# Kernel optimization log

Hardware: AMD Instinct MI355X
Metric: run time of the kernel (lower is better)

Reference implementation:

```python
import jax, jax.numpy as jnp
import numpy as np

B, H, W, DIM = 8, 128, 128, 96
MED = 2 * DIM            # med_channels
NS = 3                   # num_scales
SCTX = 48                # spatial context channels
RIN = DIM + SCTX         # reweight mlp input
RHID = int(0.25 * RIN)   # 36
ROUT = NS * MED          # 576
FH, FWH = H, W // 2 + 1  # rfft2 output grid
SCALE_HW = [(16, 9), (8, 4), (24, 13)]  # per-scale filter resolutions


def _cubic(t, a=-0.75):
    t = abs(t)
    if t <= 1.0:
        return (a + 2) * t ** 3 - (a + 3) * t ** 2 + 1.0
    if t < 2.0:
        return a * t ** 3 - 5 * a * t ** 2 + 8 * a * t - 4 * a
    return 0.0


def _resize_mat(old, new):
    # bicubic, align_corners=True, border replication (matches F.interpolate)
    M = np.zeros((new, old), dtype=np.float32)
    for j in range(new):
        s = j * (old - 1) / (new - 1) if new > 1 else 0.0
        f = int(np.floor(s))
        for k in range(-1, 3):
            M[j, min(max(f + k, 0), old - 1)] += _cubic(s - (f + k))
    return jnp.asarray(M)


def _soa(x, scale, bias):
    r = jnp.maximum(x, 0.0)
    return scale * r * r + bias


def setup_inputs() -> dict:
    key = jax.random.key(0)
    ks = jax.random.split(key, 10)
    inp = {
        "x": jax.random.normal(ks[0], (B, H, W, DIM), dtype=jnp.float32),
        "w1": jax.random.normal(ks[1], (MED, DIM), dtype=jnp.float32) * 0.02,
        "soa1_scale": jnp.ones((1,), jnp.float32),
        "soa1_bias": jnp.zeros((1,), jnp.float32),
        "cw0": jax.random.normal(ks[2], (SCALE_HW[0][0], SCALE_HW[0][1], MED, 2), dtype=jnp.float32) * 0.02,
        "cw1": jax.random.normal(ks[3], (SCALE_HW[1][0], SCALE_HW[1][1], MED, 2), dtype=jnp.float32) * 0.02,
        "cw2": jax.random.normal(ks[4], (SCALE_HW[2][0], SCALE_HW[2][1], MED, 2), dtype=jnp.float32) * 0.02,
        "sp_w": jax.random.normal(ks[5], (SCTX, DIM), dtype=jnp.float32) * 0.05,
        "bn_gamma": jnp.ones((SCTX,), jnp.float32),
        "bn_beta": jnp.zeros((SCTX,), jnp.float32),
        "bn_mean": jnp.zeros((SCTX,), jnp.float32),
        "bn_var": jnp.ones((SCTX,), jnp.float32),
        "fc1": jax.random.normal(ks[6], (RHID, RIN), dtype=jnp.float32) * 0.05,
        "mlp_scale": jnp.ones((1,), jnp.float32),
        "mlp_bias": jnp.zeros((1,), jnp.float32),
        "fc2": jax.random.normal(ks[7], (ROUT, RHID), dtype=jnp.float32) * 0.05,
        "w2": jax.random.normal(ks[8], (DIM, MED), dtype=jnp.float32) * 0.02,
    }
    return inp


def reference(x, w1, soa1_scale, soa1_bias, cw0, cw1, cw2, sp_w,
              bn_gamma, bn_beta, bn_mean, bn_var,
              fc1, mlp_scale, mlp_bias, fc2, w2):
    # pwconv1 + Soa act
    x_pre = _soa(jnp.einsum('bhwc,mc->bhwm', x, w1), soa1_scale, soa1_bias)
    # rfft2 over spatial dims (ortho) -> [B, FH, FWH, MED] complex64
    xf = jnp.fft.rfft2(x_pre.transpose(0, 3, 1, 2), axes=(2, 3), norm='ortho').transpose(0, 2, 3, 1)
    # resize each scale's complex weight to the fft grid (bicubic align_corners=True)
    filts = []
    for cw in (cw0, cw1, cw2):
        Rh = _resize_mat(cw.shape[0], FH)
        Rw = _resize_mat(cw.shape[1], FWH)
        t = jnp.einsum('Hh,hwmc->Hwmc', Rh, cw)
        t = jnp.einsum('Ww,Hwmc->HWmc', Rw, t)
        filts.append(jax.lax.complex(t[..., 0], t[..., 1]))
    filt = jnp.stack(filts)  # [NS, FH, FWH, MED] complex64
    # routing context: global channel mean + 1x1 conv / BN(eval) / relu / GAP
    gctx = x.mean(axis=(1, 2))  # [B, DIM]
    y = jnp.einsum('bhwc,sc->bhws', x, sp_w)
    y = (y - bn_mean) * jax.lax.rsqrt(bn_var + 1e-5) * bn_gamma + bn_beta
    sctx = jnp.maximum(y, 0.0).mean(axis=(1, 2))  # [B, SCTX]
    fused = jnp.concatenate([gctx, sctx], axis=1)  # [B, RIN]
    hmid = _soa(fused @ fc1.T, mlp_scale, mlp_bias)
    r = jax.nn.softmax((hmid @ fc2.T).reshape(-1, NS, MED), axis=1)  # [B, NS, MED]
    # routing-weighted combined filter + spectral multiply
    comb = jnp.einsum('shwm,bsm->bhwm', filt, r.astype(filt.dtype))
    xff = xf * comb
    xsp = jnp.fft.irfft2(xff.transpose(0, 3, 1, 2), s=(H, W), axes=(2, 3), norm='ortho').transpose(0, 2, 3, 1)
    # act2 is Identity; pwconv2
    return jnp.einsum('bhwm,cm->bhwc', xsp, w2)
```

## Files before the change

kernel.cpp:

```cpp
#include <hip/hip_runtime.h>
#include <math.h>

#define BB    8
#define HH    128
#define WW    128
#define DIM   96
#define MED   192
#define HWPX  16384
#define PSTR  16672
#define FWH   65
#define LSTR  67

#define P_OFF     0
#define P_SZ      (8*192*PSTR)
#define FILT_OFF  (P_OFF + P_SZ)
#define FILT_SZ   (3*192*128*65*2)
#define PART_OFF  (FILT_OFF + FILT_SZ)
#define PART_SZ   (8*144*256)
#define R_OFF     (PART_OFF + PART_SZ)
#define W1B_OFF   (R_OFF + 4608)
#define W2B_OFF   (W1B_OFF + 23040)

typedef __attribute__((ext_vector_type(8))) short short8_t;
typedef __attribute__((ext_vector_type(4))) float float4_t;

__device__ __forceinline__ unsigned short bf16_rne(float f){
  unsigned u = __float_as_uint(f);
  unsigned r = (u + 0x7FFFu + ((u>>16)&1u)) >> 16;
  return (unsigned short)r;
}
__device__ __forceinline__ float bf16_to_f(unsigned short h){
  return __uint_as_float(((unsigned)h) << 16);
}

__device__ __forceinline__ float cubicw(float tt){
  float t = fabsf(tt), t2=t*t, t3=t2*t;
  if (t <= 1.f) return 1.25f*t3 - 2.25f*t2 + 1.f;
  if (t < 2.f)  return -0.75f*t3 + 3.75f*t2 - 6.f*t + 3.f;
  return 0.f;
}

__global__ __launch_bounds__(256) void k_prep_filt(
    const float* __restrict__ w1, const float* __restrict__ sp_w,
    const float* __restrict__ w2,
    const float* __restrict__ cw0, const float* __restrict__ cw1,
    const float* __restrict__ cw2,
    unsigned short* __restrict__ W1B, unsigned short* __restrict__ W2B,
    float* __restrict__ filt)
{
  __shared__ float2 T[128][13];
  int bx = blockIdx.x;
  int t = threadIdx.x;

  if (bx < 36) {
    int tid = t + bx*256;
    int nthr = 256*36;
    for (int i = tid; i < 2*3*15*512; i += nthr) {
      int j = i & 7, l = (i>>3) & 63;
      int nt = (i>>9) % 15, kc = ((i>>9)/15) % 3, term = i / (3*15*512);
      int r = nt*16 + (l&15);
      int c = kc*32 + (l>>4)*8 + j;
      float v = (r < 192) ? w1[r*96 + c] : sp_w[(r-192)*96 + c];
      unsigned short hi = bf16_rne(v);
      W1B[i] = (term==0) ? hi : bf16_rne(v - bf16_to_f(hi));
    }
    for (int i = tid; i < 2*6*6*512; i += nthr) {
      int j = i & 7, l = (i>>3) & 63;
      int nt = (i>>9) % 6, kc = ((i>>9)/6) % 6, term = i / (6*6*512);
      int cp = nt*16 + (l&15);
      int m  = kc*32 + (l>>4)*8 + j;
      float v = w2[cp*192 + m];
      unsigned short hi = bf16_rne(v);
      W2B[i] = (term==0) ? hi : bf16_rne(v - bf16_to_f(hi));
    }
    return;
  }

  int fb = bx - 36;
  int s = fb / 192, m = fb - s*192;
  const float* cw = (s==0) ? cw0 : ((s==1) ? cw1 : cw2);
  const int SH = (s==0) ? 16 : ((s==1) ? 8 : 24);
  const int SW = (s==0) ? 9  : ((s==1) ? 4 : 13);

  for (int i = t; i < 128*SW; i += 256) {
    int fh = i / SW, iw = i - fh*SW;
    float sh = fh * (float)(SH-1) / 127.f;
    int fh0 = (int)floorf(sh);
    float2 acc = make_float2(0.f, 0.f);
    #pragma unroll
    for (int ka=0; ka<4; ++ka) {
      int kk = fh0-1+ka;
      float w = cubicw(sh - (float)kk);
      int ih = min(max(kk,0), SH-1);
      float2 v = *(const float2*)(cw + (size_t)((ih*SW + iw)*192 + m)*2);
      acc.x = fmaf(w, v.x, acc.x);
      acc.y = fmaf(w, v.y, acc.y);
    }
    T[fh][iw] = acc;
  }
  __syncthreads();

  float2* outp = (float2*)filt + (size_t)(s*192+m)*8320;
  for (int i = t; i < 128*65; i += 256) {
    int fh = i / 65, fw = i - fh*65;
    float sw = fw * (float)(SW-1) / 64.f;
    int fw0 = (int)floorf(sw);
    float2 acc = make_float2(0.f, 0.f);
    #pragma unroll
    for (int kb=0; kb<4; ++kb) {
      int jj = fw0-1+kb;
      float w = cubicw(sw - (float)jj);
      int iw = min(max(jj,0), SW-1);
      float2 v = T[fh][iw];
      acc.x = fmaf(w, v.x, acc.x);
      acc.y = fmaf(w, v.y, acc.y);
    }
    outp[i] = acc;
  }
}

__global__ __launch_bounds__(256) void k_pw1(
    const float* __restrict__ x, const unsigned short* __restrict__ W1B,
    const float* __restrict__ soa_scale, const float* __restrict__ soa_bias,
    const float* __restrict__ bn_gamma, const float* __restrict__ bn_beta,
    const float* __restrict__ bn_mean, const float* __restrict__ bn_var,
    float* __restrict__ P, float* __restrict__ part)
{
  __shared__ float red[4][144];
  __shared__ float bnA_s[48], bnB_s[48];
  int t = threadIdx.x;
  int lane = t & 63, wv = t >> 6;
  if (t < 48) {
    float a = bn_gamma[t] * rsqrtf(bn_var[t] + 1e-5f);
    bnA_s[t] = a; bnB_s[t] = bn_beta[t] - bn_mean[t]*a;
  }
  int blk = blockIdx.x;
  int px0 = blk*64 + wv*16;
  int b = (blk*64) >> 14;
  int pxl = px0 & 16383;
  int g = lane >> 4;

  float4_t acc[15];
  #pragma unroll
  for (int nt=0; nt<15; ++nt) acc[nt] = (float4_t){0.f,0.f,0.f,0.f};

  #pragma unroll
  for (int kc=0; kc<3; ++kc) {
    const float* xp = x + (size_t)(px0 + (lane&15))*96 + kc*32 + g*8;
    float4 v0 = *(const float4*)xp;
    float4 v1 = *(const float4*)(xp+4);
    float vv[8] = {v0.x,v0.y,v0.z,v0.w, v1.x,v1.y,v1.z,v1.w};
    #pragma unroll
    for (int j=0;j<8;j++){
      float s = vv[j];
      s += __shfl_xor(s, 1);
      s += __shfl_xor(s, 2);
      s += __shfl_xor(s, 4);
      s += __shfl_xor(s, 8);
      if ((lane & 15) == 0) red[wv][kc*32 + g*8 + j] = s;
    }
    short8_t Bh, Bl;
    #pragma unroll
    for (int j=0;j<8;j++){
      unsigned short h = bf16_rne(vv[j]);
      Bh[j] = (short)h;
      Bl[j] = (short)bf16_rne(vv[j] - bf16_to_f(h));
    }
    const short8_t* a_hi = (const short8_t*)(W1B + (size_t)(0*3+kc)*15*512) + lane;
    const short8_t* a_lo = (const short8_t*)(W1B + (size_t)(1*3+kc)*15*512) + lane;
    #pragma unroll
    for (int nt=0; nt<15; ++nt) {
      short8_t Ah = a_hi[nt*64];
      short8_t Al = a_lo[nt*64];
      acc[nt] = __builtin_amdgcn_mfma_f32_16x16x32_bf16(Ah, Bh, acc[nt], 0,0,0);
      acc[nt] = __builtin_amdgcn_mfma_f32_16x16x32_bf16(Ah, Bl, acc[nt], 0,0,0);
      acc[nt] = __builtin_amdgcn_mfma_f32_16x16x32_bf16(Al, Bh, acc[nt], 0,0,0);
    }
  }
  float sc = soa_scale[0], bi = soa_bias[0];
  #pragma unroll
  for (int nt=0; nt<12; ++nt) {
    #pragma unroll
    for (int q=0;q<4;q++){
      float d = acc[nt][q];
      float v = fmaxf(d, 0.f);
      d = sc*v*v + bi;
      int mp = nt*16 + g*4 + q;
      P[(size_t)(b*192 + mp)*PSTR + pxl + (lane&15)] = d;
    }
  }
  #pragma unroll
  for (int tile=0; tile<3; ++tile) {
    #pragma unroll
    for (int q=0;q<4;q++){
      int s = tile*16 + g*4 + q;
      float y = acc[12+tile][q];
      float v = fmaxf(bnA_s[s]*y + bnB_s[s], 0.f);
      v += __shfl_xor(v, 1);
      v += __shfl_xor(v, 2);
      v += __shfl_xor(v, 4);
      v += __shfl_xor(v, 8);
      if ((lane & 15) == 0) red[wv][96 + s] = v;
    }
  }
  __syncthreads();
  if (t < 144) {
    float s = red[0][t] + red[1][t] + red[2][t] + red[3][t];
    part[((size_t)(b*144) + t)*256 + (blk & 255)] = s;
  }
}

__global__ __launch_bounds__(256) void k_pw2(
    const float* __restrict__ P, const unsigned short* __restrict__ W2B,
    float* __restrict__ out)
{
  int t = threadIdx.x;
  int lane = t & 63, wv = t >> 6;
  int px0 = blockIdx.x*64 + wv*16;
  int b = px0 >> 14;
  int pxl = px0 & 16383;

  float4_t acc[6];
  #pragma unroll
  for (int nt=0; nt<6; ++nt) acc[nt] = (float4_t){0.f,0.f,0.f,0.f};

  #pragma unroll
  for (int kc=0; kc<6; ++kc) {
    const float* ap = P + (size_t)(b*192 + kc*32 + (lane>>4)*8)*PSTR + pxl + (lane&15);
    short8_t Ah, Al;
    #pragma unroll
    for (int j=0;j<8;j++){
      float v = ap[(size_t)j*PSTR];
      unsigned short h = bf16_rne(v);
      Ah[j] = (short)h;
      Al[j] = (short)bf16_rne(v - bf16_to_f(h));
    }
    const short8_t* b_hi = (const short8_t*)(W2B + (size_t)(0*6+kc)*6*512) + lane;
    const short8_t* b_lo = (const short8_t*)(W2B + (size_t)(1*6+kc)*6*512) + lane;
    #pragma unroll
    for (int nt=0; nt<6; ++nt) {
      short8_t Bh = b_hi[nt*64];
      short8_t Bl = b_lo[nt*64];
      acc[nt] = __builtin_amdgcn_mfma_f32_16x16x32_bf16(Ah, Bh, acc[nt], 0,0,0);
      acc[nt] = __builtin_amdgcn_mfma_f32_16x16x32_bf16(Ah, Bl, acc[nt], 0,0,0);
      acc[nt] = __builtin_amdgcn_mfma_f32_16x16x32_bf16(Al, Bh, acc[nt], 0,0,0);
    }
  }
  #pragma unroll
  for (int nt=0; nt<6; ++nt) {
    #pragma unroll
    for (int q=0;q<4;q++){
      int px = px0 + (lane>>4)*4 + q;
      out[(size_t)px*96 + nt*16 + (lane&15)] = acc[nt][q];
    }
  }
}

__global__ __launch_bounds__(256) void k_route2(
    const float* __restrict__ part,
    const float* __restrict__ fc1, const float* __restrict__ fc2,
    const float* __restrict__ mlp_scale, const float* __restrict__ mlp_bias,
    float* __restrict__ r_out)
{
  __shared__ float fused[144], hmid[36], rpre[576];
  int t = threadIdx.x, b = blockIdx.x;
  if (t < 144) {
    const float* pp = part + ((size_t)(b*144) + t)*256;
    float s = 0.f;
    for (int i = 0; i < 256; i += 4) {
      float4 v = *(const float4*)(pp + i);
      s += (v.x + v.y) + (v.z + v.w);
    }
    fused[t] = s * (1.f/16384.f);
  }
  __syncthreads();
  if (t < 36) {
    float a = 0.f;
    for (int i=0;i<144;i++) a = fmaf(fused[i], fc1[t*144+i], a);
    float rr = fmaxf(a, 0.f);
    hmid[t] = mlp_scale[0]*rr*rr + mlp_bias[0];
  }
  __syncthreads();
  for (int o = t; o < 576; o += 256) {
    float a = 0.f;
    for (int j=0;j<36;j++) a = fmaf(hmid[j], fc2[o*36+j], a);
    rpre[o] = a;
  }
  __syncthreads();
  if (t < 192) {
    float v0 = rpre[t], v1 = rpre[192+t], v2 = rpre[384+t];
    float mx = fmaxf(v0, fmaxf(v1, v2));
    float e0 = expf(v0-mx), e1 = expf(v1-mx), e2 = expf(v2-mx);
    float inv = 1.f/(e0+e1+e2);
    r_out[(b*3+0)*192+t] = e0*inv;
    r_out[(b*3+1)*192+t] = e1*inv;
    r_out[(b*3+2)*192+t] = e2*inv;
  }
}

__device__ __forceinline__ float2 c_add(float2 a, float2 b){ return make_float2(a.x+b.x, a.y+b.y); }
__device__ __forceinline__ float2 c_sub(float2 a, float2 b){ return make_float2(a.x-b.x, a.y-b.y); }
__device__ __forceinline__ float2 c_mul(float2 a, float2 w){ return make_float2(a.x*w.x - a.y*w.y, a.x*w.y + a.y*w.x); }
__device__ __forceinline__ float2 c_mulc(float2 a, float2 w){ return make_float2(a.x*w.x + a.y*w.y, a.y*w.x - a.x*w.y); }

__device__ __forceinline__ void dif4(float2* S, const float2* TW,
    int a0, int a1, int a2, int a3, int t1, int t2, int t3)
{
  float2 x0=S[a0], x1=S[a1], x2=S[a2], x3=S[a3];
  float2 u = c_add(x0,x2), d0 = c_sub(x0,x2);
  float2 s = c_add(x1,x3), d1 = c_sub(x1,x3);
  float2 w = c_mul(d0, TW[t1]);
  float2 v = c_mul(d1, TW[t2]);
  float2 t3w = TW[t3];
  S[a0] = c_add(u,s);
  S[a1] = c_mul(c_sub(u,s), t3w);
  S[a2] = c_add(w,v);
  S[a3] = c_mul(c_sub(w,v), t3w);
}

__device__ __forceinline__ void dit4(float2* S, const float2* TW,
    int a0, int a1, int a2, int a3, int tA, int tB, int tC)
{
  float2 x0=S[a0], x1=S[a1], x2=S[a2], x3=S[a3];
  float2 wA = TW[tA];
  float2 x1t = c_mulc(x1, wA), x3t = c_mulc(x3, wA);
  float2 u = c_add(x0,x1t), v = c_sub(x0,x1t);
  float2 s = c_add(x2,x3t), w = c_sub(x2,x3t);
  float2 st = c_mulc(s, TW[tB]);
  float2 wt = c_mulc(w, TW[tC]);
  S[a0] = c_add(u, st);
  S[a2] = c_sub(u, st);
  S[a1] = c_add(v, wt);
  S[a3] = c_sub(v, wt);
}

__global__ __launch_bounds__(512, 4) void k_spectral(
    float* __restrict__ P, const float* __restrict__ filt, const float* __restrict__ r)
{
  __shared__ float2 S[128*LSTR];
  __shared__ float2 TW[64];
  int t = threadIdx.x;
  int lane = t & 63, wid = t >> 6;

  int i = blockIdx.x;
  int b = (i >> 3) & 7;
  int m = (i & 7) * 24 + (i >> 6);
  float* plane = P + ((size_t)b*192 + m) * PSTR;

  {
    float ang = -6.283185307179586477f * (float)lane / 128.f;
    TW[lane] = make_float2(cosf(ang), sinf(ang));
  }

  for (int it = 0; it < 8; ++it) {
    int row = 16*wid + (lane>>5) + 2*it;
    int j   = lane & 31;
    float4 v = ((const float4*)plane)[row*32 + j];
    int base = row*LSTR + 2*j;
    S[base]   = make_float2(v.x, v.y);
    S[base+1] = make_float2(v.z, v.w);
  }
  float r0 = r[(b*3+0)*192+m];
  float r1 = r[(b*3+1)*192+m];
  float r2 = r[(b*3+2)*192+m];

  #pragma unroll
  for (int ps = 0; ps < 3; ++ps) {
    const int lh = 5 - 2*ps;
    const int h1 = 1 << lh, h2 = h1 >> 1;
    #pragma unroll
    for (int it = 0; it < 4; ++it) {
      int g = lane & 15;
      int row = 16*wid + (lane>>4) + 4*it;
      int k = g & (h2-1), blk = g >> (lh-1);
      int base = row*LSTR + blk*(2*h1) + k;
      dif4(S,TW, base, base+h2, base+h1, base+h1+h2,
           k << (6-lh), (k+h2) << (6-lh), k << (7-lh));
    }
  }

  for (int it = 0; it < 9; ++it) {
    int k   = (lane>>4) + 4*it;
    int row = 16*wid + (lane & 15);
    if (k <= 32) {
      int base = row*LSTR;
      if (k == 0) {
        float2 z = S[base];
        S[base]    = make_float2(z.x + z.y, 0.f);
        S[base+64] = make_float2(z.x - z.y, 0.f);
      } else {
        int a = __brev((unsigned)k) >> 26;
        int bidx = __brev((unsigned)(64-k)) >> 26;
        float2 A = S[base+a], B = S[base+bidx];
        float sr_ = 0.5f*(A.x+B.x), si_ = 0.5f*(A.y-B.y);
        float dr  = 0.5f*(A.x-B.x), di  = 0.5f*(A.y+B.y);
        float2 wq = TW[k];
        float tr = wq.x*di + wq.y*dr;
        float ti = -(wq.x*dr - wq.y*di);
        S[base+a]    = make_float2(sr_ + tr,  si_ + ti);
        S[base+bidx] = make_float2(sr_ - tr, -si_ + ti);
      }
    }
  }
  __syncthreads();

  #pragma unroll
  for (int ps = 0; ps < 3; ++ps) {
    const int lh = 6 - 2*ps;
    const int h1 = 1 << lh, h2 = h1 >> 1;
    for (int it = 0; it < 5; ++it) {
      int idx = t + 512*it;
      if (idx < 65*32) {
        int g = idx / 65, col = idx - g*65;
        int k = g & (h2-1), blk = g >> (lh-1);
        int p = blk*(2*h1) + k;
        dif4(S,TW, p*LSTR+col, (p+h2)*LSTR+col, (p+h1)*LSTR+col, (p+h1+h2)*LSTR+col,
             k << (6-lh), (k+h2) << (6-lh), k << (7-lh));
      }
    }
    __syncthreads();
  }

  {
    const float2* fb0 = (const float2*)filt + (size_t)(0*192+m)*8320;
    const float2* fb1 = (const float2*)filt + (size_t)(1*192+m)*8320;
    const float2* fb2 = (const float2*)filt + (size_t)(2*192+m)*8320;
    const float inv = 1.f/8192.f;
    for (int it = 0; it < 9; ++it) {
      int idx = t + 512*it;
      if (idx < 65*64) {
        int f = idx / 65, fw = idx - f*65;
        int j = __brev((unsigned)f) >> 26;
        int cc = (fw == 64) ? 64 : (__brev((unsigned)fw) >> 26);
        int a0 = (2*j)*LSTR + cc, a1 = a0 + LSTR;
        float2 u = S[a0], v = S[a1];
        float2 e = c_add(u,v), o = c_sub(u,v);
        float2 f00=fb0[idx],      f10=fb1[idx],      f20=fb2[idx];
        float2 f01=fb0[idx+4160], f11=fb1[idx+4160], f21=fb2[idx+4160];
        float cr0 = (r0*f00.x + r1*f10.x + r2*f20.x) * inv;
        float ci0 = (r0*f00.y + r1*f10.y + r2*f20.y) * inv;
        float cr1 = (r0*f01.x + r1*f11.x + r2*f21.x) * inv;
        float ci1 = (r0*f01.y + r1*f11.y + r2*f21.y) * inv;
        S[a0] = make_float2(e.x*cr0 - e.y*ci0, e.x*ci0 + e.y*cr0);
        S[a1] = make_float2(o.x*cr1 - o.y*ci1, o.x*ci1 + o.y*cr1);
      }
    }
  }
  __syncthreads();

  #pragma unroll
  for (int ps = 0; ps < 3; ++ps) {
    const int la = 2*ps;
    const int h = 1 << la;
    for (int it = 0; it < 5; ++it) {
      int idx = t + 512*it;
      if (idx < 65*32) {
        int g = idx / 65, col = idx - g*65;
        int k = g & (h-1), blk = g >> la;
        int p = blk*(4*h) + k;
        dit4(S,TW, p*LSTR+col, (p+h)*LSTR+col, (p+2*h)*LSTR+col, (p+3*h)*LSTR+col,
             k << (6-la), k << (5-la), (k+h) << (5-la));
      }
    }
    __syncthreads();
  }
  for (int it = 0; it < 9; ++it) {
    int idx = t + 512*it;
    if (idx < 65*64) {
      int k = idx / 65, col = idx - k*65;
      int a0 = k*LSTR + col, a1 = a0 + 64*LSTR;
      float2 u = S[a0], xv = S[a1];
      float2 xt = c_mulc(xv, TW[k]);
      S[a0] = c_add(u,xt); S[a1] = c_sub(u,xt);
    }
  }
  __syncthreads();

  for (int it = 0; it < 9; ++it) {
    int k   = (lane>>4) + 4*it;
    int row = 16*wid + (lane & 15);
    if (k <= 32) {
      int base = row*LSTR;
      if (k == 0) {
        float ar = S[base].x;
        float cr = S[base+64].x;
        S[base] = make_float2(0.5f*(ar+cr), 0.5f*(ar-cr));
      } else {
        int a = __brev((unsigned)k) >> 26;
        int bidx = __brev((unsigned)(64-k)) >> 26;
        float2 A = S[base+a], B = S[base+bidx];
        float sr_ = 0.5f*(A.x+B.x), si_ = 0.5f*(A.y-B.y);
        float dr  = 0.5f*(A.x-B.x), di  = 0.5f*(A.y+B.y);
        float2 wq = TW[k];
        float tr2 = wq.y*dr - wq.x*di;
        float ti2 = wq.x*dr + wq.y*di;
        S[base+a]    = make_float2(sr_ + tr2,  si_ + ti2);
        S[base+bidx] = make_float2(sr_ - tr2, -si_ + ti2);
      }
    }
  }

  #pragma unroll
  for (int ps = 0; ps < 3; ++ps) {
    const int la = 2*ps;
    const int h = 1 << la;
    #pragma unroll
    for (int it = 0; it < 4; ++it) {
      int g = lane & 15;
      int row = 16*wid + (lane>>4) + 4*it;
      int k = g & (h-1), blk = g >> la;
      int base = row*LSTR + blk*(4*h) + k;
      dit4(S,TW, base, base+h, base+2*h, base+3*h,
           k << (6-la), k << (5-la), (k+h) << (5-la));
    }
  }

  for (int it = 0; it < 8; ++it) {
    int row = 16*wid + (lane>>5) + 2*it;
    int j   = lane & 31;
    int base = row*LSTR + 2*j;
    float2 z0 = S[base], z1 = S[base+1];
    float4 v; v.x = z0.x; v.y = z0.y; v.z = z1.x; v.w = z1.y;
    ((float4*)plane)[row*32 + j] = v;
  }
}

extern "C" void kernel_launch(void* const* d_in, const int* in_sizes, int n_in,
                              void* d_out, int out_size, void* d_ws, size_t ws_size,
                              hipStream_t stream) {
  const float* x          = (const float*)d_in[0];
  const float* w1         = (const float*)d_in[1];
  const float* soa1_scale = (const float*)d_in[2];
  const float* soa1_bias  = (const float*)d_in[3];
  const float* cw0        = (const float*)d_in[4];
  const float* cw1        = (const float*)d_in[5];
  const float* cw2        = (const float*)d_in[6];
  const float* sp_w       = (const float*)d_in[7];
  const float* bn_gamma   = (const float*)d_in[8];
  const float* bn_beta    = (const float*)d_in[9];
  const float* bn_mean    = (const float*)d_in[10];
  const float* bn_var     = (const float*)d_in[11];
  const float* fc1        = (const float*)d_in[12];
  const float* mlp_scale  = (const float*)d_in[13];
  const float* mlp_bias   = (const float*)d_in[14];
  const float* fc2        = (const float*)d_in[15];
  const float* w2         = (const float*)d_in[16];
  float* out = (float*)d_out;

  float* ws   = (float*)d_ws;
  float* P    = ws + P_OFF;
  float* filt = ws + FILT_OFF;
  float* part = ws + PART_OFF;
  float* rbuf = ws + R_OFF;
  unsigned short* W1B = (unsigned short*)(ws + W1B_OFF);
  unsigned short* W2B = (unsigned short*)(ws + W2B_OFF);

  k_prep_filt<<<612, 256, 0, stream>>>(w1, sp_w, w2, cw0, cw1, cw2, W1B, W2B, filt);
  k_pw1      <<<2048,256, 0, stream>>>(x, W1B, soa1_scale, soa1_bias,
                                       bn_gamma, bn_beta, bn_mean, bn_var,
                                       P, part);
  k_route2   <<<8,   256, 0, stream>>>(part, fc1, fc2, mlp_scale, mlp_bias, rbuf);
  k_spectral <<<1536,512, 0, stream>>>(P, filt, rbuf);
  k_pw2      <<<2048,256, 0, stream>>>(P, W2B, out);
}
```

Baseline: 359.2 us.

## Split pw1 output channels across wave pairs and fuse routing MLP via last-block counter

The pw1 kernel now processes 32 pixels per block, with two waves per 16-pixel group each computing half of the 15 output tiles. This halves per-wave accumulator registers and doubles the grid, aiming for better occupancy. The separate routing kernel is removed: each block bumps an atomic counter and the last 8 blocks to finish run the routing MLP and softmax, one per batch image. This saves a launch but adds an atomic and threadfences per block. Correctness relies on the last-8 blocks seeing all partials, which is only guaranteed for the final block, so there is a possible ordering race.

```diff
diff --git a/kernel.cpp b/kernel.cpp
--- a/kernel.cpp
+++ b/kernel.cpp
@@ -11,15 +11,18 @@
 #define FWH   65
 #define LSTR  67
 
+#define PW1_GRID 4096
+
 #define P_OFF     0
 #define P_SZ      (8*192*PSTR)
 #define FILT_OFF  (P_OFF + P_SZ)
 #define FILT_SZ   (3*192*128*65*2)
 #define PART_OFF  (FILT_OFF + FILT_SZ)
-#define PART_SZ   (8*144*256)
+#define PART_SZ   (8*144*512)
 #define R_OFF     (PART_OFF + PART_SZ)
 #define W1B_OFF   (R_OFF + 4608)
 #define W2B_OFF   (W1B_OFF + 23040)
+#define CNT_OFF   (W2B_OFF + 18432)
 
 typedef __attribute__((ext_vector_type(8))) short short8_t;
 typedef __attribute__((ext_vector_type(4))) float float4_t;
@@ -46,13 +49,14 @@
     const float* __restrict__ cw0, const float* __restrict__ cw1,
     const float* __restrict__ cw2,
     unsigned short* __restrict__ W1B, unsigned short* __restrict__ W2B,
-    float* __restrict__ filt)
+    float* __restrict__ filt, int* __restrict__ cnt)
 {
   __shared__ float2 T[128][13];
   int bx = blockIdx.x;
   int t = threadIdx.x;
 
   if (bx < 36) {
+    if (bx == 0 && t == 0) *cnt = 0;
     int tid = t + bx*256;
     int nthr = 256*36;
     for (int i = tid; i < 2*3*15*512; i += nthr) {
@@ -124,25 +128,29 @@
     const float* __restrict__ soa_scale, const float* __restrict__ soa_bias,
     const float* __restrict__ bn_gamma, const float* __restrict__ bn_beta,
     const float* __restrict__ bn_mean, const float* __restrict__ bn_var,
-    float* __restrict__ P, float* __restrict__ part)
+    float* __restrict__ P, float* __restrict__ part, int* __restrict__ cnt,
+    const float* __restrict__ fc1, const float* __restrict__ fc2,
+    const float* __restrict__ mlp_scale, const float* __restrict__ mlp_bias,
+    float* __restrict__ r_out)
 {
-  __shared__ float red[4][144];
+  __shared__ float red[2][144];
   __shared__ float bnA_s[48], bnB_s[48];
   int t = threadIdx.x;
   int lane = t & 63, wv = t >> 6;
+  int pg = wv >> 1, h = wv & 1;
   if (t < 48) {
     float a = bn_gamma[t] * rsqrtf(bn_var[t] + 1e-5f);
     bnA_s[t] = a; bnB_s[t] = bn_beta[t] - bn_mean[t]*a;
   }
   int blk = blockIdx.x;
-  int px0 = blk*64 + wv*16;
-  int b = (blk*64) >> 14;
+  int px0 = blk*32 + pg*16;
+  int b = (blk*32) >> 14;
   int pxl = px0 & 16383;
   int g = lane >> 4;
 
-  float4_t acc[15];
-  #pragma unroll
-  for (int nt=0; nt<15; ++nt) acc[nt] = (float4_t){0.f,0.f,0.f,0.f};
+  float4_t acc[8];
+  #pragma unroll
+  for (int nt=0; nt<8; ++nt) acc[nt] = (float4_t){0.f,0.f,0.f,0.f};
 
   #pragma unroll
   for (int kc=0; kc<3; ++kc) {
@@ -150,63 +158,133 @@
     float4 v0 = *(const float4*)xp;
     float4 v1 = *(const float4*)(xp+4);
     float vv[8] = {v0.x,v0.y,v0.z,v0.w, v1.x,v1.y,v1.z,v1.w};
+    if (h == 0) {
+      #pragma unroll
+      for (int j=0;j<8;j++){
+        float s = vv[j];
+        s += __shfl_xor(s, 1);
+        s += __shfl_xor(s, 2);
+        s += __shfl_xor(s, 4);
+        s += __shfl_xor(s, 8);
+        if ((lane & 15) == 0) red[pg][kc*32 + g*8 + j] = s;
+      }
+    }
+    short8_t Bh, Bl;
     #pragma unroll
     for (int j=0;j<8;j++){
-      float s = vv[j];
-      s += __shfl_xor(s, 1);
-      s += __shfl_xor(s, 2);
-      s += __shfl_xor(s, 4);
-      s += __shfl_xor(s, 8);
-      if ((lane & 15) == 0) red[wv][kc*32 + g*8 + j] = s;
-    }
-    short8_t Bh, Bl;
-    #pragma unroll
-    for (int j=0;j<8;j++){
-      unsigned short h = bf16_rne(vv[j]);
-      Bh[j] = (short)h;
-      Bl[j] = (short)bf16_rne(vv[j] - bf16_to_f(h));
+      unsigned short hh = bf16_rne(vv[j]);
+      Bh[j] = (short)hh;
+      Bl[j] = (short)bf16_rne(vv[j] - bf16_to_f(hh));
     }
     const short8_t* a_hi = (const short8_t*)(W1B + (size_t)(0*3+kc)*15*512) + lane;
     const short8_t* a_lo = (const short8_t*)(W1B + (size_t)(1*3+kc)*15*512) + lane;
-    #pragma unroll
-    for (int nt=0; nt<15; ++nt) {
-      short8_t Ah = a_hi[nt*64];
-      short8_t Al = a_lo[nt*64];
-      acc[nt] = __builtin_amdgcn_mfma_f32_16x16x32_bf16(Ah, Bh, acc[nt], 0,0,0);
-      acc[nt] = __builtin_amdgcn_mfma_f32_16x16x32_bf16(Ah, Bl, acc[nt], 0,0,0);
-      acc[nt] = __builtin_amdgcn_mfma_f32_16x16x32_bf16(Al, Bh, acc[nt], 0,0,0);
+    if (h == 0) {
+      #pragma unroll
+      for (int nt=0; nt<8; ++nt) {
+        short8_t Ah = a_hi[nt*64];
+        short8_t Al = a_lo[nt*64];
+        acc[nt] = __builtin_amdgcn_mfma_f32_16x16x32_bf16(Ah, Bh, acc[nt], 0,0,0);
+        acc[nt] = __builtin_amdgcn_mfma_f32_16x16x32_bf16(Ah, Bl, acc[nt], 0,0,0);
+        acc[nt] = __builtin_amdgcn_mfma_f32_16x16x32_bf16(Al, Bh, acc[nt], 0,0,0);
+      }
+    } else {
+      #pragma unroll
+      for (int nt=0; nt<7; ++nt) {
+        short8_t Ah = a_hi[(nt+8)*64];
+        short8_t Al = a_lo[(nt+8)*64];
+        acc[nt] = __builtin_amdgcn_mfma_f32_16x16x32_bf16(Ah, Bh, acc[nt], 0,0,0);
+        acc[nt] = __builtin_amdgcn_mfma_f32_16x16x32_bf16(Ah, Bl, acc[nt], 0,0,0);
+        acc[nt] = __builtin_amdgcn_mfma_f32_16x16x32_bf16(Al, Bh, acc[nt], 0,0,0);
+      }
     }
   }
   float sc = soa_scale[0], bi = soa_bias[0];
-  #pragma unroll
-  for (int nt=0; nt<12; ++nt) {
-    #pragma unroll
-    for (int q=0;q<4;q++){
-      float d = acc[nt][q];
-      float v = fmaxf(d, 0.f);
-      d = sc*v*v + bi;
-      int mp = nt*16 + g*4 + q;
-      P[(size_t)(b*192 + mp)*PSTR + pxl + (lane&15)] = d;
-    }
-  }
-  #pragma unroll
-  for (int tile=0; tile<3; ++tile) {
-    #pragma unroll
-    for (int q=0;q<4;q++){
-      int s = tile*16 + g*4 + q;
-      float y = acc[12+tile][q];
-      float v = fmaxf(bnA_s[s]*y + bnB_s[s], 0.f);
-      v += __shfl_xor(v, 1);
-      v += __shfl_xor(v, 2);
-      v += __shfl_xor(v, 4);
-      v += __shfl_xor(v, 8);
-      if ((lane & 15) == 0) red[wv][96 + s] = v;
+  if (h == 0) {
+    #pragma unroll
+    for (int nt=0; nt<8; ++nt) {
+      #pragma unroll
+      for (int q=0;q<4;q++){
+        float d = acc[nt][q];
+        float v = fmaxf(d, 0.f);
+        d = sc*v*v + bi;
+        int mp = nt*16 + g*4 + q;
+        P[(size_t)(b*192 + mp)*PSTR + pxl + (lane&15)] = d;
+      }
+    }
+  } else {
+    #pragma unroll
+    for (int nt=0; nt<4; ++nt) {
+      #pragma unroll
+      for (int q=0;q<4;q++){
+        float d = acc[nt][q];
+        float v = fmaxf(d, 0.f);
+        d = sc*v*v + bi;
+        int mp = (nt+8)*16 + g*4 + q;
+        P[(size_t)(b*192 + mp)*PSTR + pxl + (lane&15)] = d;
+      }
+    }
+    #pragma unroll
+    for (int tile=0; tile<3; ++tile) {
+      #pragma unroll
+      for (int q=0;q<4;q++){
+        int s = tile*16 + g*4 + q;
+        float y = acc[4+tile][q];
+        float v = fmaxf(bnA_s[s]*y + bnB_s[s], 0.f);
+        v += __shfl_xor(v, 1);
+        v += __shfl_xor(v, 2);
+        v += __shfl_xor(v, 4);
+        v += __shfl_xor(v, 8);
+        if ((lane & 15) == 0) red[pg][96 + s] = v;
+      }
     }
   }
   __syncthreads();
   if (t < 144) {
-    float s = red[0][t] + red[1][t] + red[2][t] + red[3][t];
-    part[((size_t)(b*144) + t)*256 + (blk & 255)] = s;
+    float s = red[0][t] + red[1][t];
+    part[((size_t)(b*144) + t)*512 + (blk & 511)] = s;
+  }
+
+  __threadfence();
+  __shared__ int sidx;
+  if (t == 0) sidx = atomicAdd(cnt, 1);
+  __syncthreads();
+  int idx = sidx;
+  if (idx < PW1_GRID - 8) return;
+  __threadfence();
+  int b2 = idx - (PW1_GRID - 8);
+
+  __shared__ float fused[144], hmid[36], rpre[576];
+  if (t < 144) {
+    const float* pp = part + ((size_t)(b2*144) + t)*512;
+    float s = 0.f;
+    for (int i = 0; i < 512; i += 4) {
+      float4 v = *(const float4*)(pp + i);
+      s += (v.x + v.y) + (v.z + v.w);
+    }
+    fused[t] = s * (1.f/16384.f);
+  }
+  __syncthreads();
+  if (t < 36) {
+    float a = 0.f;
+    for (int i=0;i<144;i++) a = fmaf(fused[i], fc1[t*144+i], a);
+    float rr = fmaxf(a, 0.f);
+    hmid[t] = mlp_scale[0]*rr*rr + mlp_bias[0];
+  }
+  __syncthreads();
+  for (int o = t; o < 576; o += 256) {
+    float a = 0.f;
+    for (int j=0;j<36;j++) a = fmaf(hmid[j], fc2[o*36+j], a);
+    rpre[o] = a;
+  }
+  __syncthreads();
+  if (t < 192) {
+    float v0 = rpre[t], v1 = rpre[192+t], v2 = rpre[384+t];
+    float mx = fmaxf(v0, fmaxf(v1, v2));
+    float e0 = expf(v0-mx), e1 = expf(v1-mx), e2 = expf(v2-mx);
+    float inv = 1.f/(e0+e1+e2);
+    r_out[(b2*3+0)*192+t] = e0*inv;
+    r_out[(b2*3+1)*192+t] = e1*inv;
+    r_out[(b2*3+2)*192+t] = e2*inv;
   }
 }
 
@@ -253,48 +331,6 @@
       int px = px0 + (lane>>4)*4 + q;
       out[(size_t)px*96 + nt*16 + (lane&15)] = acc[nt][q];
     }
-  }
-}
-
-__global__ __launch_bounds__(256) void k_route2(
-    const float* __restrict__ part,
-    const float* __restrict__ fc1, const float* __restrict__ fc2,
-    const float* __restrict__ mlp_scale, const float* __restrict__ mlp_bias,
-    float* __restrict__ r_out)
-{
-  __shared__ float fused[144], hmid[36], rpre[576];
-  int t = threadIdx.x, b = blockIdx.x;
-  if (t < 144) {
-    const float* pp = part + ((size_t)(b*144) + t)*256;
-    float s = 0.f;
-    for (int i = 0; i < 256; i += 4) {
-      float4 v = *(const float4*)(pp + i);
-      s += (v.x + v.y) + (v.z + v.w);
-    }
-    fused[t] = s * (1.f/16384.f);
-  }
-  __syncthreads();
-  if (t < 36) {
-    float a = 0.f;
-    for (int i=0;i<144;i++) a = fmaf(fused[i], fc1[t*144+i], a);
-    float rr = fmaxf(a, 0.f);
-    hmid[t] = mlp_scale[0]*rr*rr + mlp_bias[0];
-  }
-  __syncthreads();
-  for (int o = t; o < 576; o += 256) {
-    float a = 0.f;
-    for (int j=0;j<36;j++) a = fmaf(hmid[j], fc2[o*36+j], a);
-    rpre[o] = a;
-  }
-  __syncthreads();
-  if (t < 192) {
-    float v0 = rpre[t], v1 = rpre[192+t], v2 = rpre[384+t];
-    float mx = fmaxf(v0, fmaxf(v1, v2));
-    float e0 = expf(v0-mx), e1 = expf(v1-mx), e2 = expf(v2-mx);
-    float inv = 1.f/(e0+e1+e2);
-    r_out[(b*3+0)*192+t] = e0*inv;
-    r_out[(b*3+1)*192+t] = e1*inv;
-    r_out[(b*3+2)*192+t] = e2*inv;
   }
 }
 
@@ -554,12 +590,13 @@
   float* rbuf = ws + R_OFF;
   unsigned short* W1B = (unsigned short*)(ws + W1B_OFF);
   unsigned short* W2B = (unsigned short*)(ws + W2B_OFF);
-
-  k_prep_filt<<<612, 256, 0, stream>>>(w1, sp_w, w2, cw0, cw1, cw2, W1B, W2B, filt);
-  k_pw1      <<<2048,256, 0, stream>>>(x, W1B, soa1_scale, soa1_bias,
-                                       bn_gamma, bn_beta, bn_mean, bn_var,
-                                       P, part);
-  k_route2   <<<8,   256, 0, stream>>>(part, fc1, fc2, mlp_scale, mlp_bias, rbuf);
+  int* cnt = (int*)(ws + CNT_OFF);
+
+  k_prep_filt<<<612, 256, 0, stream>>>(w1, sp_w, w2, cw0, cw1, cw2, W1B, W2B, filt, cnt);
+  k_pw1      <<<PW1_GRID, 256, 0, stream>>>(x, W1B, soa1_scale, soa1_bias,
+                                            bn_gamma, bn_beta, bn_mean, bn_var,
+                                            P, part, cnt,
+                                            fc1, fc2, mlp_scale, mlp_bias, rbuf);
   k_spectral <<<1536,512, 0, stream>>>(P, filt, rbuf);
   k_pw2      <<<2048,256, 0, stream>>>(P, W2B, out);
 }
```

Result: slower. 939.9 us (+161.7%).

## Assign FFT columns to fixed waves and drop column-FFT barriers; repack filter layout

Applied to the files above, without the earlier changes.

Column FFT passes (DIF, spectral multiply, DIT) now give each wave its own 8 columns, with the extra column 64 handled by wave 0. All of a column's butterflies therefore stay inside one wave, and the __syncthreads between passes are removed. The filter bake writes a bit-reversed, column-major float4 layout so each thread loads both spectral halves with one vector load. Relying on intra-wave ordering without barriers depends on wave-level execution semantics. Wave 0 also carries extra work for the odd column, which imbalances the waves.

```diff
diff --git a/kernel.cpp b/kernel.cpp
--- a/kernel.cpp
+++ b/kernel.cpp
@@ -14,7 +14,7 @@
 #define P_OFF     0
 #define P_SZ      (8*192*PSTR)
 #define FILT_OFF  (P_OFF + P_SZ)
-#define FILT_SZ   (3*192*128*65*2)
+#define FILT_SZ   (3*192*65*64*4)
 #define PART_OFF  (FILT_OFF + FILT_SZ)
 #define PART_SZ   (8*144*256)
 #define R_OFF     (PART_OFF + PART_SZ)
@@ -100,22 +100,28 @@
   }
   __syncthreads();
 
-  float2* outp = (float2*)filt + (size_t)(s*192+m)*8320;
-  for (int i = t; i < 128*65; i += 256) {
-    int fh = i / 65, fw = i - fh*65;
+  float4* outp = (float4*)filt + (size_t)(s*192+m)*4160;
+  for (int i = t; i < 65*64; i += 256) {
+    int cc = i >> 6, j = i & 63;
+    int f  = __brev((unsigned)j) >> 26;
+    int fw = (cc == 64) ? 64 : (__brev((unsigned)cc) >> 26);
     float sw = fw * (float)(SW-1) / 64.f;
     int fw0 = (int)floorf(sw);
-    float2 acc = make_float2(0.f, 0.f);
+    float2 a0 = make_float2(0.f, 0.f);
+    float2 a1 = make_float2(0.f, 0.f);
     #pragma unroll
     for (int kb=0; kb<4; ++kb) {
       int jj = fw0-1+kb;
       float w = cubicw(sw - (float)jj);
       int iw = min(max(jj,0), SW-1);
-      float2 v = T[fh][iw];
-      acc.x = fmaf(w, v.x, acc.x);
-      acc.y = fmaf(w, v.y, acc.y);
-    }
-    outp[i] = acc;
+      float2 v0 = T[f][iw];
+      float2 v1 = T[f+64][iw];
+      a0.x = fmaf(w, v0.x, a0.x);
+      a0.y = fmaf(w, v0.y, a0.y);
+      a1.x = fmaf(w, v1.x, a1.x);
+      a1.y = fmaf(w, v1.y, a1.y);
+    }
+    outp[i] = make_float4(a0.x, a0.y, a1.x, a1.y);
   }
 }
 
@@ -404,75 +410,100 @@
   }
   __syncthreads();
 
+  int cs = lane & 7, u8 = lane >> 3;
+  int mycol = 8*wid + cs;
+
   #pragma unroll
   for (int ps = 0; ps < 3; ++ps) {
     const int lh = 6 - 2*ps;
     const int h1 = 1 << lh, h2 = h1 >> 1;
-    for (int it = 0; it < 5; ++it) {
-      int idx = t + 512*it;
-      if (idx < 65*32) {
-        int g = idx / 65, col = idx - g*65;
-        int k = g & (h2-1), blk = g >> (lh-1);
-        int p = blk*(2*h1) + k;
-        dif4(S,TW, p*LSTR+col, (p+h2)*LSTR+col, (p+h1)*LSTR+col, (p+h1+h2)*LSTR+col,
-             k << (6-lh), (k+h2) << (6-lh), k << (7-lh));
-      }
-    }
-    __syncthreads();
+    #pragma unroll
+    for (int it = 0; it < 4; ++it) {
+      int bf = 8*it + u8;
+      int k = bf & (h2-1), blk = bf >> (lh-1);
+      int p = blk*(2*h1) + k;
+      dif4(S,TW, p*LSTR+mycol, (p+h2)*LSTR+mycol, (p+h1)*LSTR+mycol, (p+h1+h2)*LSTR+mycol,
+           k << (6-lh), (k+h2) << (6-lh), k << (7-lh));
+    }
+    if (wid == 0 && lane < 32) {
+      int bf = lane;
+      int k = bf & (h2-1), blk = bf >> (lh-1);
+      int p = blk*(2*h1) + k;
+      dif4(S,TW, p*LSTR+64, (p+h2)*LSTR+64, (p+h1)*LSTR+64, (p+h1+h2)*LSTR+64,
+           k << (6-lh), (k+h2) << (6-lh), k << (7-lh));
+    }
   }
 
   {
-    const float2* fb0 = (const float2*)filt + (size_t)(0*192+m)*8320;
-    const float2* fb1 = (const float2*)filt + (size_t)(1*192+m)*8320;
-    const float2* fb2 = (const float2*)filt + (size_t)(2*192+m)*8320;
+    const float4* fb0 = (const float4*)filt + (size_t)(0*192+m)*4160;
+    const float4* fb1 = (const float4*)filt + (size_t)(1*192+m)*4160;
+    const float4* fb2 = (const float4*)filt + (size_t)(2*192+m)*4160;
     const float inv = 1.f/8192.f;
-    for (int it = 0; it < 9; ++it) {
-      int idx = t + 512*it;
-      if (idx < 65*64) {
-        int f = idx / 65, fw = idx - f*65;
-        int j = __brev((unsigned)f) >> 26;
-        int cc = (fw == 64) ? 64 : (__brev((unsigned)fw) >> 26);
-        int a0 = (2*j)*LSTR + cc, a1 = a0 + LSTR;
-        float2 u = S[a0], v = S[a1];
-        float2 e = c_add(u,v), o = c_sub(u,v);
-        float2 f00=fb0[idx],      f10=fb1[idx],      f20=fb2[idx];
-        float2 f01=fb0[idx+4160], f11=fb1[idx+4160], f21=fb2[idx+4160];
-        float cr0 = (r0*f00.x + r1*f10.x + r2*f20.x) * inv;
-        float ci0 = (r0*f00.y + r1*f10.y + r2*f20.y) * inv;
-        float cr1 = (r0*f01.x + r1*f11.x + r2*f21.x) * inv;
-        float ci1 = (r0*f01.y + r1*f11.y + r2*f21.y) * inv;
-        S[a0] = make_float2(e.x*cr0 - e.y*ci0, e.x*ci0 + e.y*cr0);
-        S[a1] = make_float2(o.x*cr1 - o.y*ci1, o.x*ci1 + o.y*cr1);
-      }
-    }
-  }
-  __syncthreads();
+    #pragma unroll
+    for (int it = 0; it < 8; ++it) {
+      int j = 8*it + u8;
+      int a0 = (2*j)*LSTR + mycol, a1 = a0 + LSTR;
+      float2 uu = S[a0], vv = S[a1];
+      float2 e = c_add(uu,vv), o = c_sub(uu,vv);
+      int fi = mycol*64 + j;
+      float4 q0 = fb0[fi], q1 = fb1[fi], q2 = fb2[fi];
+      float cr0 = (r0*q0.x + r1*q1.x + r2*q2.x) * inv;
+      float ci0 = (r0*q0.y + r1*q1.y + r2*q2.y) * inv;
+      float cr1 = (r0*q0.z + r1*q1.z + r2*q2.z) * inv;
+      float ci1 = (r0*q0.w + r1*q1.w + r2*q2.w) * inv;
+      S[a0] = make_float2(e.x*cr0 - e.y*ci0, e.x*ci0 + e.y*cr0);
+      S[a1] = make_float2(o.x*cr1 - o.y*ci1, o.x*ci1 + o.y*cr1);
+    }
+    if (wid == 0) {
+      int j = lane;
+      int a0 = (2*j)*LSTR + 64, a1 = a0 + LSTR;
+      float2 uu = S[a0], vv = S[a1];
+      float2 e = c_add(uu,vv), o = c_sub(uu,vv);
+      int fi = 64*64 + j;
+      float4 q0 = fb0[fi], q1 = fb1[fi], q2 = fb2[fi];
+      float cr0 = (r0*q0.x + r1*q1.x + r2*q2.x) * inv;
+      float ci0 = (r0*q0.y + r1*q1.y + r2*q2.y) * inv;
+      float cr1 = (r0*q0.z + r1*q1.z + r2*q2.z) * inv;
+      float ci1 = (r0*q0.w + r1*q1.w + r2*q2.w) * inv;
+      S[a0] = make_float2(e.x*cr0 - e.y*ci0, e.x*ci0 + e.y*cr0);
+      S[a1] = make_float2(o.x*cr1 - o.y*ci1, o.x*ci1 + o.y*cr1);
+    }
+  }
 
   #pragma unroll
   for (int ps = 0; ps < 3; ++ps) {
     const int la = 2*ps;
     const int h = 1 << la;
-    for (int it = 0; it < 5; ++it) {
-      int idx = t + 512*it;
-      if (idx < 65*32) {
-        int g = idx / 65, col = idx - g*65;
-        int k = g & (h-1), blk = g >> la;
-        int p = blk*(4*h) + k;
-        dit4(S,TW, p*LSTR+col, (p+h)*LSTR+col, (p+2*h)*LSTR+col, (p+3*h)*LSTR+col,
-             k << (6-la), k << (5-la), (k+h) << (5-la));
-      }
-    }
-    __syncthreads();
-  }
-  for (int it = 0; it < 9; ++it) {
-    int idx = t + 512*it;
-    if (idx < 65*64) {
-      int k = idx / 65, col = idx - k*65;
-      int a0 = k*LSTR + col, a1 = a0 + 64*LSTR;
-      float2 u = S[a0], xv = S[a1];
-      float2 xt = c_mulc(xv, TW[k]);
-      S[a0] = c_add(u,xt); S[a1] = c_sub(u,xt);
-    }
+    #pragma unroll
+    for (int it = 0; it < 4; ++it) {
+      int bf = 8*it + u8;
+      int k = bf & (h-1), blk = bf >> la;
+      int p = blk*(4*h) + k;
+      dit4(S,TW, p*LSTR+mycol, (p+h)*LSTR+mycol, (p+2*h)*LSTR+mycol, (p+3*h)*LSTR+mycol,
+           k << (6-la), k << (5-la), (k+h) << (5-la));
+    }
+    if (wid == 0 && lane < 32) {
+      int bf = lane;
+      int k = bf & (h-1), blk = bf >> la;
+      int p = blk*(4*h) + k;
+      dit4(S,TW, p*LSTR+64, (p+h)*LSTR+64, (p+2*h)*LSTR+64, (p+3*h)*LSTR+64,
+           k << (6-la), k << (5-la), (k+h) << (5-la));
+    }
+  }
+  #pragma unroll
+  for (int it = 0; it < 8; ++it) {
+    int k = 8*it + u8;
+    int a0 = k*LSTR + mycol, a1 = a0 + 64*LSTR;
+    float2 uu = S[a0], xv = S[a1];
+    float2 xt = c_mulc(xv, TW[k]);
+    S[a0] = c_add(uu,xt); S[a1] = c_sub(uu,xt);
+  }
+  if (wid == 0) {
+    int k = lane;
+    int a0 = k*LSTR + 64, a1 = a0 + 64*LSTR;
+    float2 uu = S[a0], xv = S[a1];
+    float2 xt = c_mulc(xv, TW[k]);
+    S[a0] = c_add(uu,xt); S[a1] = c_sub(uu,xt);
   }
   __syncthreads();
 
```

Result: no change. 357.7 us (-0.4%).
